# Kernel tuning notes

Measured on AMD Instinct MI355X. Metric: run time of the kernel, lower is better.

The kernel has to match this reference:

```python
import jax, jax.numpy as jnp
import numpy as np

EMBED_DIM = 1024
NUM_HEADS = 16
HEAD_DIM = EMBED_DIM // NUM_HEADS


def setup_inputs() -> dict:
    key = jax.random.key(0)
    ks = jax.random.split(key, 11)
    B, N, C = 2, 2048, EMBED_DIM
    s = 1.0 / np.sqrt(C)
    return {
        "query": jax.random.normal(ks[0], (B, N, C), jnp.float32),
        "key": jax.random.normal(ks[1], (B, N, C), jnp.float32),
        "value": jax.random.normal(ks[2], (B, N, C), jnp.float32),
        # torch nn.Linear weights: [out_features, in_features]
        "Wq": jax.random.normal(ks[3], (C, C), jnp.float32) * s,
        "bq": jnp.zeros((C,), jnp.float32),
        "Wk": jax.random.normal(ks[4], (C, C), jnp.float32) * s,
        "bk": jnp.zeros((C,), jnp.float32),
        "Wv": jax.random.normal(ks[5], (C, C), jnp.float32) * s,
        "bv": jnp.zeros((C,), jnp.float32),
        "Wo": jax.random.normal(ks[6], (C, C), jnp.float32) * s,
        "bo": jnp.zeros((C,), jnp.float32),
    }


def reference(query, key, value, Wq, bq, Wk, bk, Wv, bv, Wo, bo):
    B, N, C = query.shape
    H, D = NUM_HEADS, HEAD_DIM
    # projections (torch Linear: x @ W.T + b)
    q = query @ Wq.T + bq
    k = key @ Wk.T + bk
    v = value @ Wv.T + bv
    # [B, N, C] -> [B, H, N, D]
    q = q.reshape(B, N, H, D).transpose(0, 2, 1, 3)
    k = k.reshape(B, N, H, D).transpose(0, 2, 1, 3)
    v = v.reshape(B, N, H, D).transpose(0, 2, 1, 3)
    # scores: [B, H, N, N]
    scores = jnp.einsum("bhqd,bhkd->bhqk", q, k) / jnp.sqrt(jnp.asarray(D, q.dtype))
    attn = jax.nn.softmax(scores, axis=-1)
    # attend: [B, H, N, D] -> [B, N, C]
    out = jnp.einsum("bhqk,bhkd->bhqd", attn, v)
    out = out.transpose(0, 2, 1, 3).reshape(B, N, C)
    return out @ Wo.T + bo
```

## Files before the change

kernel.cpp:

```cpp
#include <hip/hip_runtime.h>
#include <hip/hip_bf16.h>
#include <cstdint>

typedef short bf16x8 __attribute__((ext_vector_type(8)));
typedef float f32x4 __attribute__((ext_vector_type(4)));
typedef float f32x16 __attribute__((ext_vector_type(16)));
typedef uint32_t u32x4v __attribute__((ext_vector_type(4)));
typedef unsigned short u16;

#define BATCH 2
#define NTOK 2048
#define CDIM 1024
#define NHEAD 16
#define DHEAD 64
#define MROWS 4096
#define KDIM 1024
#define KVB 64
#define NT (NTOK / KVB)

__device__ __forceinline__ u16 f2bf(float x) {
    uint32_t b = __float_as_uint(x);
    uint32_t r = (b + 0x7fffu + ((b >> 16) & 1u)) >> 16;
    return (u16)r;
}

__device__ __forceinline__ uint32_t packbf2(float lo, float hi) {
    float2 f; f.x = lo; f.y = hi;
    __hip_bfloat162 h = __float22bfloat162_rn(f);
    uint32_t r;
    __builtin_memcpy(&r, &h, 4);
    return r;
}

__device__ __forceinline__ void gload_lds16(const void* g, void* l) {
    __builtin_amdgcn_global_load_lds((const __attribute__((address_space(1))) void*)g,
                                     (__attribute__((address_space(3))) void*)l,
                                     16, 0, 0);
}

__global__ __launch_bounds__(256) void cast_kernel(
    const float* __restrict__ q, const float* __restrict__ k, const float* __restrict__ v,
    const float* __restrict__ wq, const float* __restrict__ wk, const float* __restrict__ wv,
    const float* __restrict__ wo, u16* __restrict__ dst) {
    const size_t TOT = 16u << 20;
    size_t i0 = ((size_t)blockIdx.x * 256 + threadIdx.x) * 4;
    size_t stride = (size_t)gridDim.x * 256 * 4;
    for (size_t i = i0; i < TOT; i += stride) {
        const float* src;
        size_t off = i;
        if (i < (4u << 20))        { src = q;  }
        else if (i < (8u << 20))   { src = k;  off = i - (4u << 20); }
        else if (i < (12u << 20))  { src = v;  off = i - (8u << 20); }
        else if (i < (13u << 20))  { src = wq; off = i - (12u << 20); }
        else if (i < (14u << 20))  { src = wk; off = i - (13u << 20); }
        else if (i < (15u << 20))  { src = wv; off = i - (14u << 20); }
        else                       { src = wo; off = i - (15u << 20); }
        float4 f = *(const float4*)(src + off);
        u16 o0 = f2bf(f.x), o1 = f2bf(f.y), o2 = f2bf(f.z), o3 = f2bf(f.w);
        uint2 packed;
        packed.x = (uint32_t)o0 | ((uint32_t)o1 << 16);
        packed.y = (uint32_t)o2 | ((uint32_t)o3 << 16);
        *(uint2*)(dst + i) = packed;
    }
}

__global__ __launch_bounds__(256, 3) void gemm_qkv(
    const u16* __restrict__ Xq, const u16* __restrict__ Xk, const u16* __restrict__ Xv,
    const u16* __restrict__ Wq, const u16* __restrict__ Wk, const u16* __restrict__ Wv,
    const float* __restrict__ bq, const float* __restrict__ bk, const float* __restrict__ bv,
    u16* __restrict__ Qo, u16* __restrict__ Ko, u16* __restrict__ Vo) {
    __shared__ u16 sA[128 * 32];
    __shared__ u16 sB[128 * 32];
    const int tid = threadIdx.x;
    const int lane = tid & 63;
    const int wave = tid >> 6;
    const int z = blockIdx.z;
    const u16* A  = (z == 0) ? Xq : (z == 1) ? Xk : Xv;
    const u16* Bw = (z == 0) ? Wq : (z == 1) ? Wk : Wv;
    const float* bias = (z == 0) ? bq : (z == 1) ? bk : bv;
    u16* Out = (z == 0) ? Qo : (z == 1) ? Ko : Vo;
    const float scale = (z == 0) ? 0.125f * 1.44269504088896f : 1.0f;

    const int m0 = blockIdx.x * 128, n0 = blockIdx.y * 128;
    const int wm = (wave >> 1) * 64, wn = (wave & 1) * 64;
    f32x4 acc[4][4] = {};
    const int rsel = lane & 15;
    const int ksel = (lane >> 4) * 8;

    for (int k0 = 0; k0 < KDIM; k0 += 32) {
#pragma unroll
        for (int u = 0; u < 2; ++u) {
            int c = tid + u * 256;
            int row = c >> 2, cin = c & 3;
            gload_lds16(A + (size_t)(m0 + row) * KDIM + k0 + cin * 8, &sA[c * 8]);
            gload_lds16(Bw + (size_t)(n0 + row) * KDIM + k0 + cin * 8, &sB[c * 8]);
        }
        __syncthreads();
        bf16x8 af[4], bfr[4];
#pragma unroll
        for (int i = 0; i < 4; ++i)
            af[i] = *(const bf16x8*)&sA[(wm + i * 16 + rsel) * 32 + ksel];
#pragma unroll
        for (int j = 0; j < 4; ++j)
            bfr[j] = *(const bf16x8*)&sB[(wn + j * 16 + rsel) * 32 + ksel];
#pragma unroll
        for (int i = 0; i < 4; ++i)
#pragma unroll
            for (int j = 0; j < 4; ++j)
                acc[i][j] = __builtin_amdgcn_mfma_f32_16x16x32_bf16(af[i], bfr[j], acc[i][j], 0, 0, 0);
        __syncthreads();
    }

    if (z != 2) {
#pragma unroll
        for (int i = 0; i < 4; ++i) {
            int mbase = m0 + wm + i * 16 + (lane >> 4) * 4;
#pragma unroll
            for (int j = 0; j < 4; ++j) {
                int n = n0 + wn + j * 16 + (lane & 15);
                float bv2 = bias[n];
                int h = n >> 6, d = n & 63;
#pragma unroll
                for (int r = 0; r < 4; ++r) {
                    int m = mbase + r;
                    int b = m >> 11, tok = m & 2047;
                    Out[(((size_t)(b * NHEAD + h)) * NTOK + tok) * DHEAD + d] =
                        f2bf((acc[i][j][r] + bv2) * scale);
                }
            }
        }
    } else {
#pragma unroll
        for (int i = 0; i < 4; ++i) {
            int mbase = m0 + wm + i * 16 + (lane >> 4) * 4;
            int b = mbase >> 11, tok = mbase & 2047;
#pragma unroll
            for (int j = 0; j < 4; ++j) {
                int n = n0 + wn + j * 16 + (lane & 15);
                float bv2 = bias[n];
                int h = n >> 6, d = n & 63;
                uint2 st;
                st.x = packbf2(acc[i][j][0] + bv2, acc[i][j][1] + bv2);
                st.y = packbf2(acc[i][j][2] + bv2, acc[i][j][3] + bv2);
                *(uint2*)&Out[(((size_t)(b * NHEAD + h)) * DHEAD + d) * NTOK + tok] = st;
            }
        }
    }
}

__global__ __launch_bounds__(256, 3) void gemm_out(
    const u16* __restrict__ A,
    const u16* __restrict__ Bw,
    const float* __restrict__ bias,
    float* __restrict__ Out,
    int M, int N, int K) {
    __shared__ u16 sA[128 * 32];
    __shared__ u16 sB[128 * 32];
    const int tid = threadIdx.x;
    const int lane = tid & 63;
    const int wave = tid >> 6;
    const int m0 = blockIdx.x * 128, n0 = blockIdx.y * 128;
    const int wm = (wave >> 1) * 64, wn = (wave & 1) * 64;
    f32x4 acc[4][4] = {};
    const int rsel = lane & 15;
    const int ksel = (lane >> 4) * 8;

    for (int k0 = 0; k0 < K; k0 += 32) {
#pragma unroll
        for (int u = 0; u < 2; ++u) {
            int c = tid + u * 256;
            int row = c >> 2, cin = c & 3;
            gload_lds16(A + (size_t)(m0 + row) * K + k0 + cin * 8, &sA[c * 8]);
            gload_lds16(Bw + (size_t)(n0 + row) * K + k0 + cin * 8, &sB[c * 8]);
        }
        __syncthreads();
        bf16x8 af[4], bfr[4];
#pragma unroll
        for (int i = 0; i < 4; ++i)
            af[i] = *(const bf16x8*)&sA[(wm + i * 16 + rsel) * 32 + ksel];
#pragma unroll
        for (int j = 0; j < 4; ++j)
            bfr[j] = *(const bf16x8*)&sB[(wn + j * 16 + rsel) * 32 + ksel];
#pragma unroll
        for (int i = 0; i < 4; ++i)
#pragma unroll
            for (int j = 0; j < 4; ++j)
                acc[i][j] = __builtin_amdgcn_mfma_f32_16x16x32_bf16(af[i], bfr[j], acc[i][j], 0, 0, 0);
        __syncthreads();
    }

#pragma unroll
    for (int i = 0; i < 4; ++i) {
        int mbase = m0 + wm + i * 16 + (lane >> 4) * 4;
#pragma unroll
        for (int j = 0; j < 4; ++j) {
            int n = n0 + wn + j * 16 + (lane & 15);
            float bv = bias[n];
#pragma unroll
            for (int r = 0; r < 4; ++r) {
                int m = mbase + r;
                Out[(size_t)m * N + n] = acc[i][j][r] + bv;
            }
        }
    }
}

__global__ __launch_bounds__(256, 2) void attn_kernel(
    const u16* __restrict__ Qg, const u16* __restrict__ Kg, const u16* __restrict__ Vg,
    u16* __restrict__ Og) {
    __shared__ u16 Ks[2][KVB * 64];
    __shared__ u16 Vt[2][64 * KVB];
    const int tid = threadIdx.x, lane = tid & 63, wave = tid >> 6;
    const int hi = lane >> 5, lq = lane & 31;

    int flat = blockIdx.x;
    int vflat = (flat & 7) * 64 + (flat >> 3);
    int bh = vflat >> 4;
    int qtile = vflat & 15;

    const int h = bh & (NHEAD - 1), b = bh >> 4;
    const u16* Qh = Qg + (size_t)bh * NTOK * DHEAD;
    const u16* Kh = Kg + (size_t)bh * NTOK * DHEAD;
    const u16* VhT = Vg + (size_t)bh * DHEAD * NTOK;
    const int qrow0 = qtile * 128 + wave * 32;
    const int qr = qrow0 + lq;

    bf16x8 qf[4];
#pragma unroll
    for (int dk = 0; dk < 4; ++dk)
        qf[dk] = *(const bf16x8*)&Qh[(size_t)qr * DHEAD + dk * 16 + hi * 8];

    f32x16 acc0 = {}, acc1 = {};
    float mrun = -1e30f, lrun = 0.f;

    const int pr = ((lq >> 2) & 1) * 8 + (lq & 3) + ((lq >> 3) & 1) * 4 + (lq >> 4) * 16;

    {
#pragma unroll
        for (int u = 0; u < 2; ++u) {
            int c2 = tid + u * 256;
            int kv = c2 >> 3, gi = c2 & 7;
            gload_lds16(Kh + (size_t)kv * DHEAD + (gi ^ (kv & 7)) * 8, &Ks[0][c2 * 8]);
        }
#pragma unroll
        for (int u = 0; u < 2; ++u) {
            int c2 = tid + u * 256;
            int d = c2 >> 3, gi = c2 & 7;
            gload_lds16(VhT + (size_t)d * NTOK + (gi ^ (d & 7)) * 8, &Vt[0][c2 * 8]);
        }
    }
    __syncthreads();

    int cur = 0;
    for (int t = 0; t < NT; ++t) {
        const bool pre = (t + 1 < NT);
        if (pre) {
#pragma unroll
            for (int u = 0; u < 2; ++u) {
                int c2 = tid + u * 256;
                int kv = c2 >> 3, gi = c2 & 7;
                gload_lds16(Kh + (size_t)((t + 1) * KVB + kv) * DHEAD + (gi ^ (kv & 7)) * 8,
                            &Ks[cur ^ 1][c2 * 8]);
            }
#pragma unroll
            for (int u = 0; u < 2; ++u) {
                int c2 = tid + u * 256;
                int d = c2 >> 3, gi = c2 & 7;
                gload_lds16(VhT + (size_t)d * NTOK + (t + 1) * KVB + (gi ^ (d & 7)) * 8,
                            &Vt[cur ^ 1][c2 * 8]);
            }
        }

        f32x16 T0 = {}, T1 = {};
        const char* kb_ = (const char*)&Ks[cur][0];
        __builtin_amdgcn_s_setprio(1);
#pragma unroll
        for (int dk = 0; dk < 4; ++dk) {
            int x = dk * 32 + hi * 16;
            int kv0 = pr, kv1 = 32 + pr;
            bf16x8 k0 = *(const bf16x8*)(kb_ + kv0 * 128 + (x ^ ((kv0 & 7) << 4)));
            bf16x8 k1 = *(const bf16x8*)(kb_ + kv1 * 128 + (x ^ ((kv1 & 7) << 4)));
            T0 = __builtin_amdgcn_mfma_f32_32x32x16_bf16(k0, qf[dk], T0, 0, 0, 0);
            T1 = __builtin_amdgcn_mfma_f32_32x32x16_bf16(k1, qf[dk], T1, 0, 0, 0);
        }
        __builtin_amdgcn_s_setprio(0);

        float m16[16];
#pragma unroll
        for (int i = 0; i < 16; ++i) m16[i] = fmaxf(T0[i], T1[i]);
#pragma unroll
        for (int s2 = 8; s2 >= 1; s2 >>= 1)
#pragma unroll
            for (int i = 0; i < s2; ++i) m16[i] = fmaxf(m16[i], m16[i + s2]);
        float mx = fmaxf(m16[0], __shfl_xor(m16[0], 32));

        if (mx > mrun + 11.0f) {
            float scl = __builtin_amdgcn_exp2f(mrun - mx);
            mrun = mx;
            lrun *= scl;
            acc0 *= scl;
            acc1 *= scl;
        }

        float p0[16], p1[16];
#pragma unroll
        for (int i = 0; i < 16; ++i) {
            p0[i] = __builtin_amdgcn_exp2f(T0[i] - mrun);
            p1[i] = __builtin_amdgcn_exp2f(T1[i] - mrun);
        }

        bf16x8 pf[4];
#pragma unroll
        for (int kb2 = 0; kb2 < 2; ++kb2) {
            const float* pp = kb2 ? p1 : p0;
#pragma unroll
            for (int hh = 0; hh < 2; ++hh) {
                int rb = hh * 8;
                u32x4v w = { packbf2(pp[rb + 0], pp[rb + 1]),
                             packbf2(pp[rb + 2], pp[rb + 3]),
                             packbf2(pp[rb + 4], pp[rb + 5]),
                             packbf2(pp[rb + 6], pp[rb + 7]) };
                pf[kb2 * 2 + hh] = *(bf16x8*)&w;
            }
        }

        const char* vb_ = (const char*)&Vt[cur][0];
        __builtin_amdgcn_s_setprio(1);
#pragma unroll
        for (int db = 0; db < 2; ++db) {
            int d = db * 32 + lq;
#pragma unroll
            for (int ks = 0; ks < 4; ++ks) {
                int off = d * 128 + ((ks * 32 + hi * 16) ^ ((d & 7) << 4));
                bf16x8 vf = *(const bf16x8*)(vb_ + off);
                if (db == 0)
                    acc0 = __builtin_amdgcn_mfma_f32_32x32x16_bf16(vf, pf[ks], acc0, 0, 0, 0);
                else
                    acc1 = __builtin_amdgcn_mfma_f32_32x32x16_bf16(vf, pf[ks], acc1, 0, 0, 0);
            }
        }
        __builtin_amdgcn_s_setprio(0);

        float sm[16];
#pragma unroll
        for (int i = 0; i < 16; ++i) sm[i] = p0[i] + p1[i];
#pragma unroll
        for (int s2 = 8; s2 >= 1; s2 >>= 1)
#pragma unroll
            for (int i = 0; i < s2; ++i) sm[i] += sm[i + s2];
        lrun += sm[0] + __shfl_xor(sm[0], 32);

        __syncthreads();
        cur ^= 1;
    }

    float rinv = 1.0f / lrun;
#pragma unroll
    for (int db = 0; db < 2; ++db) {
#pragma unroll
        for (int rq = 0; rq < 4; ++rq) {
            int based = db * 32 + 8 * rq + 4 * hi;
            float o0, o1, o2, o3;
            if (db == 0) {
                o0 = acc0[rq * 4 + 0]; o1 = acc0[rq * 4 + 1];
                o2 = acc0[rq * 4 + 2]; o3 = acc0[rq * 4 + 3];
            } else {
                o0 = acc1[rq * 4 + 0]; o1 = acc1[rq * 4 + 1];
                o2 = acc1[rq * 4 + 2]; o3 = acc1[rq * 4 + 3];
            }
            uint2 st;
            st.x = packbf2(o0 * rinv, o1 * rinv);
            st.y = packbf2(o2 * rinv, o3 * rinv);
            *(uint2*)&Og[((size_t)(b * NTOK + qr)) * CDIM + h * DHEAD + based] = st;
        }
    }
}

extern "C" void kernel_launch(void* const* d_in, const int* in_sizes, int n_in,
                              void* d_out, int out_size, void* d_ws, size_t ws_size,
                              hipStream_t stream) {
    const float* q  = (const float*)d_in[0];
    const float* k  = (const float*)d_in[1];
    const float* v  = (const float*)d_in[2];
    const float* Wq = (const float*)d_in[3];
    const float* bq = (const float*)d_in[4];
    const float* Wk = (const float*)d_in[5];
    const float* bk = (const float*)d_in[6];
    const float* Wv = (const float*)d_in[7];
    const float* bv = (const float*)d_in[8];
    const float* Wo = (const float*)d_in[9];
    const float* bo = (const float*)d_in[10];

    u16* wsp = (u16*)d_ws;
    u16* Xq  = wsp;
    u16* Xk  = Xq + (4u << 20);
    u16* Xv  = Xk + (4u << 20);
    u16* Wqb = Xv + (4u << 20);
    u16* Wkb = Wqb + (1u << 20);
    u16* Wvb = Wkb + (1u << 20);
    u16* Wob = Wvb + (1u << 20);
    u16* Qb  = Wob + (1u << 20);
    u16* Kb  = Qb + (4u << 20);
    u16* Vb  = Kb + (4u << 20);
    u16* Ab  = Xq;

    cast_kernel<<<2048, 256, 0, stream>>>(q, k, v, Wq, Wk, Wv, Wo, Xq);

    gemm_qkv<<<dim3(MROWS / 128, CDIM / 128, 3), 256, 0, stream>>>(
        Xq, Xk, Xv, Wqb, Wkb, Wvb, bq, bk, bv, Qb, Kb, Vb);

    attn_kernel<<<512, 256, 0, stream>>>(Qb, Kb, Vb, Ab);

    gemm_out<<<dim3(MROWS / 128, CDIM / 128), 256, 0, stream>>>(
        Ab, Wob, bo, (float*)d_out, MROWS, CDIM, KDIM);
}
```

Before: 133.9 us.

## Double attention KV tile to 128 and make softmax rescale wave-uniform

```diff
diff --git a/kernel.cpp b/kernel.cpp
--- a/kernel.cpp
+++ b/kernel.cpp
@@ -15,7 +15,7 @@
 #define DHEAD 64
 #define MROWS 4096
 #define KDIM 1024
-#define KVB 64
+#define KVB 128
 #define NT (NTOK / KVB)
 
 __device__ __forceinline__ u16 f2bf(float x) {
@@ -231,22 +231,22 @@
         qf[dk] = *(const bf16x8*)&Qh[(size_t)qr * DHEAD + dk * 16 + hi * 8];
 
     f32x16 acc0 = {}, acc1 = {};
-    float mrun = -1e30f, lrun = 0.f;
+    float mrun = 0.f, lrun = 0.f;
 
     const int pr = ((lq >> 2) & 1) * 8 + (lq & 3) + ((lq >> 3) & 1) * 4 + (lq >> 4) * 16;
 
     {
 #pragma unroll
-        for (int u = 0; u < 2; ++u) {
+        for (int u = 0; u < 4; ++u) {
             int c2 = tid + u * 256;
             int kv = c2 >> 3, gi = c2 & 7;
             gload_lds16(Kh + (size_t)kv * DHEAD + (gi ^ (kv & 7)) * 8, &Ks[0][c2 * 8]);
         }
 #pragma unroll
-        for (int u = 0; u < 2; ++u) {
+        for (int u = 0; u < 4; ++u) {
             int c2 = tid + u * 256;
-            int d = c2 >> 3, gi = c2 & 7;
-            gload_lds16(VhT + (size_t)d * NTOK + (gi ^ (d & 7)) * 8, &Vt[0][c2 * 8]);
+            int d = c2 >> 4, gi = c2 & 15;
+            gload_lds16(VhT + (size_t)d * NTOK + (gi ^ (d & 15)) * 8, &Vt[0][c2 * 8]);
         }
     }
     __syncthreads();
@@ -256,71 +256,72 @@
         const bool pre = (t + 1 < NT);
         if (pre) {
 #pragma unroll
-            for (int u = 0; u < 2; ++u) {
+            for (int u = 0; u < 4; ++u) {
                 int c2 = tid + u * 256;
                 int kv = c2 >> 3, gi = c2 & 7;
                 gload_lds16(Kh + (size_t)((t + 1) * KVB + kv) * DHEAD + (gi ^ (kv & 7)) * 8,
                             &Ks[cur ^ 1][c2 * 8]);
             }
 #pragma unroll
-            for (int u = 0; u < 2; ++u) {
+            for (int u = 0; u < 4; ++u) {
                 int c2 = tid + u * 256;
-                int d = c2 >> 3, gi = c2 & 7;
-                gload_lds16(VhT + (size_t)d * NTOK + (t + 1) * KVB + (gi ^ (d & 7)) * 8,
+                int d = c2 >> 4, gi = c2 & 15;
+                gload_lds16(VhT + (size_t)d * NTOK + (t + 1) * KVB + (gi ^ (d & 15)) * 8,
                             &Vt[cur ^ 1][c2 * 8]);
             }
         }
 
-        f32x16 T0 = {}, T1 = {};
+        f32x16 T[4] = {};
         const char* kb_ = (const char*)&Ks[cur][0];
         __builtin_amdgcn_s_setprio(1);
 #pragma unroll
         for (int dk = 0; dk < 4; ++dk) {
             int x = dk * 32 + hi * 16;
-            int kv0 = pr, kv1 = 32 + pr;
-            bf16x8 k0 = *(const bf16x8*)(kb_ + kv0 * 128 + (x ^ ((kv0 & 7) << 4)));
-            bf16x8 k1 = *(const bf16x8*)(kb_ + kv1 * 128 + (x ^ ((kv1 & 7) << 4)));
-            T0 = __builtin_amdgcn_mfma_f32_32x32x16_bf16(k0, qf[dk], T0, 0, 0, 0);
-            T1 = __builtin_amdgcn_mfma_f32_32x32x16_bf16(k1, qf[dk], T1, 0, 0, 0);
+#pragma unroll
+            for (int j = 0; j < 4; ++j) {
+                int kv = j * 32 + pr;
+                bf16x8 kf = *(const bf16x8*)(kb_ + kv * 128 + (x ^ ((kv & 7) << 4)));
+                T[j] = __builtin_amdgcn_mfma_f32_32x32x16_bf16(kf, qf[dk], T[j], 0, 0, 0);
+            }
         }
         __builtin_amdgcn_s_setprio(0);
 
         float m16[16];
 #pragma unroll
-        for (int i = 0; i < 16; ++i) m16[i] = fmaxf(T0[i], T1[i]);
+        for (int i = 0; i < 16; ++i)
+            m16[i] = fmaxf(fmaxf(T[0][i], T[1][i]), fmaxf(T[2][i], T[3][i]));
 #pragma unroll
         for (int s2 = 8; s2 >= 1; s2 >>= 1)
 #pragma unroll
             for (int i = 0; i < s2; ++i) m16[i] = fmaxf(m16[i], m16[i + s2]);
-        float mx = fmaxf(m16[0], __shfl_xor(m16[0], 32));
-
-        if (mx > mrun + 11.0f) {
-            float scl = __builtin_amdgcn_exp2f(mrun - mx);
-            mrun = mx;
+        float mx = m16[0];
+
+        if (__any(mx > mrun + 11.0f)) {
+            float mxf = fmaxf(mx, __shfl_xor(mx, 32));
+            float scl = __builtin_amdgcn_exp2f(mrun - mxf);
+            mrun = mxf;
             lrun *= scl;
             acc0 *= scl;
             acc1 *= scl;
         }
 
-        float p0[16], p1[16];
-#pragma unroll
-        for (int i = 0; i < 16; ++i) {
-            p0[i] = __builtin_amdgcn_exp2f(T0[i] - mrun);
-            p1[i] = __builtin_amdgcn_exp2f(T1[i] - mrun);
-        }
-
-        bf16x8 pf[4];
-#pragma unroll
-        for (int kb2 = 0; kb2 < 2; ++kb2) {
-            const float* pp = kb2 ? p1 : p0;
+#pragma unroll
+        for (int j = 0; j < 4; ++j)
+#pragma unroll
+            for (int i = 0; i < 16; ++i)
+                T[j][i] = __builtin_amdgcn_exp2f(T[j][i] - mrun);
+
+        bf16x8 pf[8];
+#pragma unroll
+        for (int j = 0; j < 4; ++j) {
 #pragma unroll
             for (int hh = 0; hh < 2; ++hh) {
                 int rb = hh * 8;
-                u32x4v w = { packbf2(pp[rb + 0], pp[rb + 1]),
-                             packbf2(pp[rb + 2], pp[rb + 3]),
-                             packbf2(pp[rb + 4], pp[rb + 5]),
-                             packbf2(pp[rb + 6], pp[rb + 7]) };
-                pf[kb2 * 2 + hh] = *(bf16x8*)&w;
+                u32x4v w = { packbf2(T[j][rb + 0], T[j][rb + 1]),
+                             packbf2(T[j][rb + 2], T[j][rb + 3]),
+                             packbf2(T[j][rb + 4], T[j][rb + 5]),
+                             packbf2(T[j][rb + 6], T[j][rb + 7]) };
+                pf[j * 2 + hh] = *(bf16x8*)&w;
             }
         }
 
@@ -330,8 +331,8 @@
         for (int db = 0; db < 2; ++db) {
             int d = db * 32 + lq;
 #pragma unroll
-            for (int ks = 0; ks < 4; ++ks) {
-                int off = d * 128 + ((ks * 32 + hi * 16) ^ ((d & 7) << 4));
+            for (int ks = 0; ks < 8; ++ks) {
+                int off = d * 256 + ((ks * 32 + hi * 16) ^ ((d & 15) << 4));
                 bf16x8 vf = *(const bf16x8*)(vb_ + off);
                 if (db == 0)
                     acc0 = __builtin_amdgcn_mfma_f32_32x32x16_bf16(vf, pf[ks], acc0, 0, 0, 0);
@@ -343,7 +344,8 @@
 
         float sm[16];
 #pragma unroll
-        for (int i = 0; i < 16; ++i) sm[i] = p0[i] + p1[i];
+        for (int i = 0; i < 16; ++i)
+            sm[i] = (T[0][i] + T[1][i]) + (T[2][i] + T[3][i]);
 #pragma unroll
         for (int s2 = 8; s2 >= 1; s2 >>= 1)
 #pragma unroll
```

Result: faster. 130.3 us (-2.7%).
